# Kernel optimization log

Measured on AMD Instinct MI355X. Metric: run time of the kernel, lower is better.

## Reference

```python
import jax, jax.numpy as jnp
import numpy as np

B, T, D, H, L = 32, 1024, 512, 512, 2  # batch, time, input dim, rnn_dim, layers


def setup_inputs() -> dict:
    key = jax.random.key(0)
    ks = jax.random.split(key, 4)
    x = jax.random.normal(ks[0], (B, T, D), jnp.float32)
    # contiguous-length mask like Keras masking (True = valid timestep)
    lengths = jax.random.randint(ks[1], (B,), T // 4, T + 1)
    mask = jnp.arange(T)[None, :] < lengths[:, None]
    s = 1.0 / np.sqrt(H)
    Wk = jax.random.normal(ks[2], (L, 2, D, 4 * H), jnp.float32) * s  # input kernels [layer, dir]
    Wr = jax.random.normal(ks[3], (L, 2, H, 4 * H), jnp.float32) * s  # recurrent kernels
    b = jnp.zeros((L, 2, 4 * H), jnp.float32)
    return {"x": x, "mask": mask, "Wk": Wk, "Wr": Wr, "b": b}


def _lstm_dir(x, mask, Wk, Wr, b, reverse):
    """Single-direction Keras-style LSTM with masking (masked steps carry h,c)."""
    if reverse:  # Bidirectional backward layer: process reversed time, reverse output back
        x = x[:, ::-1]
        mask = mask[:, ::-1]
    # precompute input projection for all timesteps: [B,T,4H]
    xw = jnp.einsum('btd,dg->btg', x, Wk) + b
    h0 = jnp.zeros((x.shape[0], Wr.shape[0]), x.dtype)

    def step(carry, inp):
        h, c = carry
        xw_t, m_t = inp  # [B,4H], [B]
        z = xw_t + h @ Wr
        i, f, g, o = jnp.split(z, 4, axis=-1)  # Keras gate order i,f,c,o
        c_new = jax.nn.sigmoid(f) * c + jax.nn.sigmoid(i) * jnp.tanh(g)
        h_new = jax.nn.sigmoid(o) * jnp.tanh(c_new)
        m = m_t[:, None]
        h = jnp.where(m, h_new, h)  # masked step: copy previous output/state
        c = jnp.where(m, c_new, c)
        return (h, c), h

    _, ys = jax.lax.scan(step, (h0, h0), (xw.transpose(1, 0, 2), mask.T))
    ys = ys.transpose(1, 0, 2)  # [B,T,H]
    if reverse:
        ys = ys[:, ::-1]
    return ys


def reference(x, mask, Wk, Wr, b):
    inp = x
    for l in range(L):
        fwd = _lstm_dir(inp, mask, Wk[l, 0], Wr[l, 0], b[l, 0], False)
        bwd = _lstm_dir(inp, mask, Wk[l, 1], Wr[l, 1], b[l, 1], True)
        res = fwd + bwd  # merge_mode='sum'
        inp = res + inp if l > 0 else res  # residual from layer 1 onward
    return inp
```

## Files before the change

### kernel.cpp

```cpp
#include <hip/hip_runtime.h>
#include <stdint.h>


#define B_ 32
#define T_ 1024
#define H_ 512
#define G_ 2048

typedef _Float16 f16;
typedef _Float16 f16x8 __attribute__((ext_vector_type(8)));
typedef float f32x16 __attribute__((ext_vector_type(16)));

#define AL_U(p) __hip_atomic_load((p), __ATOMIC_RELAXED, __HIP_MEMORY_SCOPE_AGENT)
#define AS_U(p, v) __hip_atomic_store((p), (v), __ATOMIC_RELAXED, __HIP_MEMORY_SCOPE_AGENT)
#define AADD_U(p, v) __hip_atomic_fetch_add((p), (v), __ATOMIC_RELAXED, __HIP_MEMORY_SCOPE_AGENT)

struct Claim {
  unsigned cnt[8];
  unsigned dirclaim;
  int xcddir[8];
  unsigned pad[15];
};

__device__ __forceinline__ float sigm(float x) { return 1.f / (1.f + __expf(-x)); }
__device__ __forceinline__ float tanh_(float x) { return 1.f - 2.f / (__expf(2.f * x) + 1.f); }

__global__ void cvt_x_t(const float* __restrict__ x, f16* __restrict__ xh) {
  size_t j = (size_t)blockIdx.x * 256 + threadIdx.x;
  int b = (int)(j >> 16);
  int t = (int)((j >> 6) & 1023);
  int d0 = (int)(j & 63) * 8;
  const float4* p = (const float4*)(x + ((size_t)b * T_ + t) * H_ + d0);
  float4 a = p[0], c = p[1];
  union { f16 h[8]; uint4 u; } r;
  r.h[0] = (f16)a.x; r.h[1] = (f16)a.y; r.h[2] = (f16)a.z; r.h[3] = (f16)a.w;
  r.h[4] = (f16)c.x; r.h[5] = (f16)c.y; r.h[6] = (f16)c.z; r.h[7] = (f16)c.w;
  size_t o = (((size_t)t * 32 + (d0 >> 4)) * 32 + b) * 16 + (d0 & 15);
  *(uint4*)(xh + o) = r.u;
}

__global__ void cvt_w(const float* __restrict__ W, f16* __restrict__ Wb) {
  const int wgi = blockIdx.x, z = blockIdx.y;
  const int tid = threadIdx.x;
  const float* src = W + (size_t)z * H_ * G_;
  __shared__ unsigned short st[512];
  for (int cp = 0; cp < 2; ++cp)
    for (int ks = 0; ks < 32; ++ks) {
      size_t cbase = ((((size_t)z * 32 + wgi) * 2 + cp) * 32 + ks) * 512;
#pragma unroll
      for (int pass = 0; pass < 2; ++pass) {
        int e = tid + pass * 256;
        int col = e & 31, kk = e >> 5;
        int gc = (2 * cp + (col >> 4)) * 512 + wgi * 16 + (col & 15);
        f16 v = (f16)src[(size_t)(ks * 16 + kk) * G_ + gc];
        st[col * 16 + kk] = __builtin_bit_cast(unsigned short, v);
      }
      __syncthreads();
      unsigned pk = (unsigned)st[2 * tid] | ((unsigned)st[2 * tid + 1] << 16);
      *((unsigned*)(Wb + cbase) + tid) = pk;
      __syncthreads();
    }
}

__global__ void sum_h(const f16* __restrict__ a, const f16* __restrict__ b,
                      f16* __restrict__ r) {
  size_t i = ((size_t)blockIdx.x * 256 + threadIdx.x) * 8;
  f16x8 va = *(const f16x8*)(a + i), vb = *(const f16x8*)(b + i);
  *(f16x8*)(r + i) = va + vb;
}

template <int LAYER>
__global__ __attribute__((amdgpu_flat_work_group_size(512, 512),
                          amdgpu_waves_per_eu(2, 2)))
void lstm_rec10(
    const f16* __restrict__ xh,
    const f16* __restrict__ wkb,
    const f16* __restrict__ wrb,
    const float* __restrict__ biasAll,
    const void* __restrict__ maskp,
    f16* __restrict__ ring,
    unsigned* __restrict__ flags,
    Claim* __restrict__ cl,
    f16* __restrict__ hout,
    float* __restrict__ out,
    const f16* __restrict__ res1h)
{
  const int tid = threadIdx.x, wave = tid >> 6, lane = tid & 63;

  __shared__ int s_dir, s_wgi;
  __shared__ float zbuf[2][4][32][48];
  __shared__ char lds_pad[33024];

  lds_pad[tid] = (char)tid;
  {
    char pv = ((volatile char*)lds_pad)[(tid * 37) & 32767];
    asm volatile("" :: "v"((int)pv));
  }

  if (tid == 0) {
    unsigned xcd;
    asm volatile("s_getreg_b32 %0, hwreg(HW_REG_XCC_ID)" : "=s"(xcd));
    xcd &= 7u;
    unsigned slot = AADD_U(&cl->cnt[xcd], 1u);
    int dir = -1, wgi = -1;
    if (slot < 32u) {
      if (slot == 31u) {
        unsigned d = AADD_U(&cl->dirclaim, 1u);
        int val = (d < 2u) ? (int)(d + 1u) : -1;
        __hip_atomic_store(&cl->xcddir[xcd], val, __ATOMIC_RELAXED, __HIP_MEMORY_SCOPE_AGENT);
      }
      while (true) {
        int v = __hip_atomic_load(&cl->xcddir[xcd], __ATOMIC_RELAXED, __HIP_MEMORY_SCOPE_AGENT);
        if (v != 0) { if (v > 0) { dir = v - 1; wgi = (int)slot; } break; }
        if (AL_U(&cl->dirclaim) >= 2u && AL_U(&cl->cnt[xcd]) < 32u) break;
        __builtin_amdgcn_s_sleep(2);
      }
    }
    s_dir = dir; s_wgi = wgi;
  }
  __syncthreads();
  const int dir = s_dir, wgi = s_wgi;
  if (dir < 0) return;

  const int cp = wave & 1, kq = wave >> 1;
  const int j0 = wgi * 16;
  const int z = LAYER * 2 + dir;
  const int laneA = (lane & 31) * 16 + (lane >> 5) * 8;
  const int hi = lane >> 5;

  const f16* wkc = wkb + ((((size_t)z * 32 + wgi) * 2 + cp) * 32 + kq * 8) * 512;
  const f16* wrc = wrb + ((((size_t)z * 32 + wgi) * 2 + cp) * 32 + kq * 8) * 512;
  f16x8 wfk[8], wfr[8];
#pragma unroll
  for (int i = 0; i < 8; ++i) {
    wfk[i] = *(const f16x8*)(wkc + i * 512 + laneA);
    wfr[i] = *(const f16x8*)(wrc + i * 512 + laneA);
  }
#pragma unroll
  for (int i = 0; i < 8; ++i) {
    asm volatile("" : "+v"(wfk[i]));
    asm volatile("" : "+v"(wfr[i]));
  }

  const int cb = tid >> 4, cj = tid & 15;
  const float* bb = biasAll + (size_t)z * G_;
  float bias4[4];
#pragma unroll
  for (int g = 0; g < 4; ++g) bias4[g] = bb[g * H_ + j0 + cj];

  const unsigned char* mbytes = (const unsigned char*)maskp;
  const unsigned* mwords = (const unsigned*)maskp;
  const bool bytelay = (mbytes[1] != 0);

  float hstate = 0.f, cstate = 0.f;
  unsigned* flagd = flags + (size_t)dir * T_ * 32;
  const f32x16 vzero = {0.f};

  for (int s = 0; s < T_; ++s) {
    const int t = dir ? (T_ - 1 - s) : s;
    const f16* xb = xh + (size_t)t * 16384 + (size_t)kq * 8 * 512 + laneA;
    f32x16 acc = vzero;
    {
      f16x8 xf[8];
#pragma unroll
      for (int i = 0; i < 8; ++i) xf[i] = *(const f16x8*)(xb + i * 512);
#pragma unroll
      for (int i = 0; i < 8; ++i)
        acc = __builtin_amdgcn_mfma_f32_32x32x16_f16(xf[i], wfk[i], acc, 0, 0, 0);
    }
    const size_t btm = (size_t)cb * T_ + t;
    const bool mv = bytelay ? (mbytes[btm] != 0) : (mwords[btm] != 0);
    float xr = 0.f;
    if (LAYER == 1 && dir == 0)
      xr = (float)res1h[(((size_t)t * 32 + wgi) * 32 + cb) * 16 + cj];

    if (s > 0) {
      if (wave == 0) {
        const unsigned* fl = flagd + (size_t)(s - 1) * 32 + (lane & 31);
        while (true) {
          unsigned v = AL_U(fl);
          if (__ballot(v == 1u) == ~0ull) break;
        }
      }
      __syncthreads();
      const f16* hb = ring + ((size_t)dir * 16 + ((s - 1) & 15)) * 16384 +
                      (size_t)kq * 8 * 512 + laneA;
      f16x8 hf[8];
#pragma unroll
      for (int i = 0; i < 8; ++i) hf[i] = *(const f16x8*)(hb + i * 512);
#pragma unroll
      for (int i = 0; i < 8; ++i)
        acc = __builtin_amdgcn_mfma_f32_32x32x16_f16(hf[i], wfr[i], acc, 0, 0, 0);
    }
#pragma unroll
    for (int r = 0; r < 16; ++r) {
      int row = (r & 3) + 8 * (r >> 2) + 4 * hi;
      zbuf[cp][kq][row][lane & 31] = acc[r];
    }
    __syncthreads();

    float zi = zbuf[0][0][cb][cj] + zbuf[0][1][cb][cj] + zbuf[0][2][cb][cj] + zbuf[0][3][cb][cj] + bias4[0];
    float zf = zbuf[0][0][cb][16 + cj] + zbuf[0][1][cb][16 + cj] + zbuf[0][2][cb][16 + cj] + zbuf[0][3][cb][16 + cj] + bias4[1];
    float zg = zbuf[1][0][cb][cj] + zbuf[1][1][cb][cj] + zbuf[1][2][cb][cj] + zbuf[1][3][cb][cj] + bias4[2];
    float zo = zbuf[1][0][cb][16 + cj] + zbuf[1][1][cb][16 + cj] + zbuf[1][2][cb][16 + cj] + zbuf[1][3][cb][16 + cj] + bias4[3];
    float ig = sigm(zi), fg = sigm(zf), gg = tanh_(zg), og = sigm(zo);
    float cn = fg * cstate + ig * gg;
    float hn = og * tanh_(cn);
    if (mv) { cstate = cn; hstate = hn; }

    f16 h16 = (f16)hstate;
    unsigned short hu = __builtin_bit_cast(unsigned short, h16);
    unsigned ob = (unsigned)__shfl_xor((int)hu, 1);
    unsigned pk = (unsigned)hu | ((ob & 0xffffu) << 16);
    if ((cj & 1) == 0) {
      f16* pb = ring + ((size_t)dir * 16 + (s & 15)) * 16384;
      *(unsigned*)(pb + (size_t)wgi * 512 + cb * 16 + cj) = pk;
    }
    asm volatile("s_waitcnt vmcnt(0)" ::: "memory");
    __syncthreads();
    if (tid == 0) AS_U(&flagd[(size_t)s * 32 + wgi], 1u);

    if (LAYER == 0) {
      if ((cj & 1) == 0) {
        f16* hx = hout + ((size_t)dir * T_ + t) * 16384;
        __builtin_nontemporal_store(pk, (unsigned*)(hx + (size_t)wgi * 512 + cb * 16 + cj));
      }
    } else {
      atomicAdd(&out[btm * H_ + j0 + cj], hstate + xr);
    }
  }
}

extern "C" void kernel_launch(void* const* d_in, const int* in_sizes, int n_in,
                              void* d_out, int out_size, void* d_ws, size_t ws_size,
                              hipStream_t stream) {
  const float* x = (const float*)d_in[0];
  const void* maskp = (const void*)d_in[1];
  const float* Wk = (const float*)d_in[2];
  const float* Wr = (const float*)d_in[3];
  const float* bias = (const float*)d_in[4];
  float* out = (float*)d_out;
  (void)in_sizes; (void)n_in;

  char* ws = (char*)d_ws;
  f16* xh = (f16*)(ws);
  f16* wkb = (f16*)(ws + 33554432ull);
  f16* wrb = (f16*)(ws + 41943040ull);
  unsigned* flags0 = (unsigned*)(ws + 50331648ull);
  unsigned* flags1 = (unsigned*)(ws + 50593792ull);
  Claim* cl0 = (Claim*)(ws + 50855936ull);
  Claim* cl1 = (Claim*)(ws + 50856960ull);
  f16* ring = (f16*)(ws + 50857984ull);
  if (ws_size < 51906560ull) return;

  f16* hf = (f16*)d_out;
  f16* hb = (f16*)d_out + (size_t)T_ * 16384;

  hipError_t e0 = hipMemsetAsync(flags0, 0, 526336ull, stream);
  (void)e0;
  cvt_x_t<<<8192, 256, 0, stream>>>(x, xh);
  cvt_w<<<dim3(32, 4), 256, 0, stream>>>(Wk, wkb);
  cvt_w<<<dim3(32, 4), 256, 0, stream>>>(Wr, wrb);

  lstm_rec10<0><<<512, 512, 0, stream>>>(xh, wkb, wrb, bias, maskp, ring, flags0,
                                         cl0, hf, (float*)nullptr, (const f16*)nullptr);
  sum_h<<<8192, 256, 0, stream>>>(hf, hb, xh);

  hipError_t e1 = hipMemsetAsync(d_out, 0, 67108864ull, stream);
  (void)e1;
  lstm_rec10<1><<<512, 512, 0, stream>>>(xh, wkb, wrb, bias, maskp, ring, flags1,
                                         cl1, (f16*)nullptr, out, xh);
}
```

Baseline: 6.365 ms.

## Stage recurrent weights in LDS and batch per-step output stores every 8 steps

New measurement: 6.480 ms. About the same (+1.8%).

```diff
diff --git a/kernel.cpp b/kernel.cpp
--- a/kernel.cpp
+++ b/kernel.cpp
@@ -72,7 +72,7 @@
 template <int LAYER>
 __global__ __attribute__((amdgpu_flat_work_group_size(512, 512),
                           amdgpu_waves_per_eu(2, 2)))
-void lstm_rec10(
+void lstm_rec11(
     const f16* __restrict__ xh,
     const f16* __restrict__ wkb,
     const f16* __restrict__ wrb,
@@ -89,13 +89,8 @@
 
   __shared__ int s_dir, s_wgi;
   __shared__ float zbuf[2][4][32][48];
-  __shared__ char lds_pad[33024];
-
-  lds_pad[tid] = (char)tid;
-  {
-    char pv = ((volatile char*)lds_pad)[(tid * 37) & 32767];
-    asm volatile("" :: "v"((int)pv));
-  }
+  __shared__ f16 wrl[2][4][8][512];
+  __shared__ unsigned obuf[8][512];
 
   if (tid == 0) {
     unsigned xcd;
@@ -128,19 +123,20 @@
   const int laneA = (lane & 31) * 16 + (lane >> 5) * 8;
   const int hi = lane >> 5;
 
+  {
+    const uint4* src = (const uint4*)(wrb + (size_t)(z * 32 + wgi) * 32768);
+    uint4* dst = (uint4*)wrl;
+#pragma unroll
+    for (int r = 0; r < 8; ++r) dst[r * 512 + tid] = src[r * 512 + tid];
+  }
   const f16* wkc = wkb + ((((size_t)z * 32 + wgi) * 2 + cp) * 32 + kq * 8) * 512;
-  const f16* wrc = wrb + ((((size_t)z * 32 + wgi) * 2 + cp) * 32 + kq * 8) * 512;
-  f16x8 wfk[8], wfr[8];
-#pragma unroll
-  for (int i = 0; i < 8; ++i) {
-    wfk[i] = *(const f16x8*)(wkc + i * 512 + laneA);
-    wfr[i] = *(const f16x8*)(wrc + i * 512 + laneA);
-  }
-#pragma unroll
-  for (int i = 0; i < 8; ++i) {
-    asm volatile("" : "+v"(wfk[i]));
-    asm volatile("" : "+v"(wfr[i]));
-  }
+  f16x8 wfk[8];
+#pragma unroll
+  for (int i = 0; i < 8; ++i) wfk[i] = *(const f16x8*)(wkc + i * 512 + laneA);
+#pragma unroll
+  for (int i = 0; i < 8; ++i) asm volatile("" : "+v"(wfk[i]));
+
+  const f16* wr_lds = &wrl[cp][kq][0][0];
 
   const int cb = tid >> 4, cj = tid & 15;
   const float* bb = biasAll + (size_t)z * G_;
@@ -155,9 +151,28 @@
   float hstate = 0.f, cstate = 0.f;
   unsigned* flagd = flags + (size_t)dir * T_ * 32;
   const f32x16 vzero = {0.f};
+  __syncthreads();
 
   for (int s = 0; s < T_; ++s) {
     const int t = dir ? (T_ - 1 - s) : s;
+
+    if ((s & 7) == 0 && s > 0) {
+#pragma unroll
+      for (int jj = 0; jj < 8; ++jj) {
+        int sj = s - 8 + jj;
+        int tj = dir ? (T_ - 1 - sj) : sj;
+        unsigned pv = obuf[jj][tid];
+        if (LAYER == 0) {
+          if ((cj & 1) == 0)
+            __builtin_nontemporal_store(pv,
+              (unsigned*)(hout + ((size_t)dir * T_ + tj) * 16384 + (size_t)wgi * 512 + cb * 16 + cj));
+        } else {
+          atomicAdd(&out[((size_t)cb * T_ + tj) * H_ + j0 + cj],
+                    __builtin_bit_cast(float, pv));
+        }
+      }
+    }
+
     const f16* xb = xh + (size_t)t * 16384 + (size_t)kq * 8 * 512 + laneA;
     f32x16 acc = vzero;
     {
@@ -168,8 +183,8 @@
       for (int i = 0; i < 8; ++i)
         acc = __builtin_amdgcn_mfma_f32_32x32x16_f16(xf[i], wfk[i], acc, 0, 0, 0);
     }
-    const size_t btm = (size_t)cb * T_ + t;
-    const bool mv = bytelay ? (mbytes[btm] != 0) : (mwords[btm] != 0);
+    const bool mv = bytelay ? (mbytes[(size_t)cb * T_ + t] != 0)
+                            : (mwords[(size_t)cb * T_ + t] != 0);
     float xr = 0.f;
     if (LAYER == 1 && dir == 0)
       xr = (float)res1h[(((size_t)t * 32 + wgi) * 32 + cb) * 16 + cj];
@@ -185,12 +200,12 @@
       __syncthreads();
       const f16* hb = ring + ((size_t)dir * 16 + ((s - 1) & 15)) * 16384 +
                       (size_t)kq * 8 * 512 + laneA;
-      f16x8 hf[8];
-#pragma unroll
-      for (int i = 0; i < 8; ++i) hf[i] = *(const f16x8*)(hb + i * 512);
-#pragma unroll
-      for (int i = 0; i < 8; ++i)
-        acc = __builtin_amdgcn_mfma_f32_32x32x16_f16(hf[i], wfr[i], acc, 0, 0, 0);
+#pragma unroll
+      for (int i = 0; i < 8; ++i) {
+        f16x8 hf = *(const f16x8*)(hb + i * 512);
+        f16x8 wr = *(const f16x8*)(wr_lds + i * 512 + laneA);
+        acc = __builtin_amdgcn_mfma_f32_32x32x16_f16(hf, wr, acc, 0, 0, 0);
+      }
     }
 #pragma unroll
     for (int r = 0; r < 16; ++r) {
@@ -216,17 +231,25 @@
       f16* pb = ring + ((size_t)dir * 16 + (s & 15)) * 16384;
       *(unsigned*)(pb + (size_t)wgi * 512 + cb * 16 + cj) = pk;
     }
+    obuf[s & 7][tid] = (LAYER == 0) ? pk : __builtin_bit_cast(unsigned, hstate + xr);
+
     asm volatile("s_waitcnt vmcnt(0)" ::: "memory");
     __syncthreads();
     if (tid == 0) AS_U(&flagd[(size_t)s * 32 + wgi], 1u);
-
+  }
+
+#pragma unroll
+  for (int jj = 0; jj < 8; ++jj) {
+    int sj = T_ - 8 + jj;
+    int tj = dir ? (T_ - 1 - sj) : sj;
+    unsigned pv = obuf[jj][tid];
     if (LAYER == 0) {
-      if ((cj & 1) == 0) {
-        f16* hx = hout + ((size_t)dir * T_ + t) * 16384;
-        __builtin_nontemporal_store(pk, (unsigned*)(hx + (size_t)wgi * 512 + cb * 16 + cj));
-      }
+      if ((cj & 1) == 0)
+        __builtin_nontemporal_store(pv,
+          (unsigned*)(hout + ((size_t)dir * T_ + tj) * 16384 + (size_t)wgi * 512 + cb * 16 + cj));
     } else {
-      atomicAdd(&out[btm * H_ + j0 + cj], hstate + xr);
+      atomicAdd(&out[((size_t)cb * T_ + tj) * H_ + j0 + cj],
+                __builtin_bit_cast(float, pv));
     }
   }
 }
@@ -262,12 +285,12 @@
   cvt_w<<<dim3(32, 4), 256, 0, stream>>>(Wk, wkb);
   cvt_w<<<dim3(32, 4), 256, 0, stream>>>(Wr, wrb);
 
-  lstm_rec10<0><<<512, 512, 0, stream>>>(xh, wkb, wrb, bias, maskp, ring, flags0,
+  lstm_rec11<0><<<512, 512, 0, stream>>>(xh, wkb, wrb, bias, maskp, ring, flags0,
                                          cl0, hf, (float*)nullptr, (const f16*)nullptr);
   sum_h<<<8192, 256, 0, stream>>>(hf, hb, xh);
 
   hipError_t e1 = hipMemsetAsync(d_out, 0, 67108864ull, stream);
   (void)e1;
-  lstm_rec10<1><<<512, 512, 0, stream>>>(xh, wkb, wrb, bias, maskp, ring, flags1,
+  lstm_rec11<1><<<512, 512, 0, stream>>>(xh, wkb, wrb, bias, maskp, ring, flags1,
                                          cl1, (f16*)nullptr, out, xh);
 }
```
